# Kernel tuning notes

Hardware: AMD Instinct MI355X
Metric: run time of the kernel (lower is better)

The kernel has to match this reference:

```python
import jax, jax.numpy as jnp
from jax import lax
import numpy as np

PN_FEAT = 64


def _conv(x, w, b):
    # x: [B,H,W,Cin], w: [kh,kw,Cin,Cout] (SAME padding, stride 1)
    return lax.conv_general_dilated(x, w, (1, 1), 'SAME',
                                    dimension_numbers=('NHWC', 'HWIO', 'NHWC')) + b


def setup_inputs() -> dict:
    key = jax.random.key(0)
    ks = jax.random.split(key, 12)
    B, P, N, C = 4, 5000, 100, 8
    nx = ny = 240
    pillars = jax.random.normal(ks[0], (B, P, N, C), dtype=jnp.float32)
    pillar_idxs = jax.random.randint(ks[1], (B, P, 2), 0, nx).astype(jnp.int32)
    def lin(k, fi, fo):
        return jax.random.normal(k, (fi, fo), dtype=jnp.float32) / np.sqrt(fi).astype(np.float32)
    def cnv(k, kh, kw, ci, co):
        return jax.random.normal(k, (kh, kw, ci, co), dtype=jnp.float32) / np.sqrt(kh * kw * ci).astype(np.float32)
    return {
        'pillars': pillars,
        'pillar_idxs': pillar_idxs,
        'nx': nx,
        'ny': ny,
        # pointnet MLP: 8 -> 64 (tanh) -> 64
        'pn_w0': lin(ks[2], 8, 64), 'pn_b0': jnp.zeros((64,), jnp.float32),
        'pn_w1': lin(ks[3], 64, PN_FEAT), 'pn_b1': jnp.zeros((PN_FEAT,), jnp.float32),
        # resnet costmap CNN: 64 -> 128 (tanh) -> 128 (tanh) -> 1, relu output
        'cw0': cnv(ks[4], 3, 3, PN_FEAT, 128), 'cb0': jnp.zeros((128,), jnp.float32),
        'cw1': cnv(ks[5], 3, 3, 128, 128), 'cb1': jnp.zeros((128,), jnp.float32),
        'cw2': cnv(ks[6], 1, 1, 128, 1), 'cb2': jnp.zeros((1,), jnp.float32),
    }


def reference(pillars, pillar_idxs, nx, ny,
              pn_w0, pn_b0, pn_w1, pn_b1,
              cw0, cb0, cw1, cb1, cw2, cb2):
    VALID_THRESH = 1000000.0
    ACT_SCALE = 1.0
    # mask padded points (norm >= 1e6 means invalid)
    valid = (jnp.linalg.norm(pillars, axis=-1, keepdims=True) < VALID_THRESH).astype(pillars.dtype)
    # per-point MLP: [B,P,N,8] -> [B,P,N,F]
    h = jnp.tanh(pillars @ pn_w0 + pn_b0)
    feat = h @ pn_w1 + pn_b1
    # masked max over points in each pillar -> [B,P,F]
    pmax = jnp.max(feat * valid, axis=-2)
    # scatter pillar features into BEV pseudo-image [B,nx,ny,F]
    B = pillars.shape[0]
    bidx = jnp.arange(B)[:, None]                      # [B,1]
    img = jnp.zeros((B, nx, ny, PN_FEAT), pillars.dtype)
    img = img.at[bidx, pillar_idxs[..., 0], pillar_idxs[..., 1]].set(pmax)
    # costmap CNN head (NHWC internally; original is NCHW, same math)
    x = jnp.tanh(_conv(img, cw0, cb0))
    x = jnp.tanh(_conv(x, cw1, cb1))
    x = _conv(x, cw2, cb2)
    return jax.nn.relu(x) * ACT_SCALE            # [B,nx,ny,1]
```

## Files before the change

### kernel.cpp

```cpp
#include <hip/hip_runtime.h>
#include <hip/hip_bf16.h>
#include <math.h>

#define B  4
#define P  5000
#define NPT 100
#define F  64
#define NX 240
#define NY 240
#define C1 128

typedef __attribute__((ext_vector_type(8)))  short short8;
typedef __attribute__((ext_vector_type(16))) float f32x16;

__device__ __forceinline__ float tanh_fast(float x) {
    float e = exp2f(x * 2.8853900817779268f);
    float r = __builtin_amdgcn_rcpf(e + 1.0f);
    return __builtin_fmaf(-2.0f, r, 1.0f);
}
__device__ __forceinline__ short bf16_bits(float f) {
    return (short)(__bfloat16_as_ushort(__float2bfloat16(f)));
}
__device__ __forceinline__ void async_load16(const void* g, void* l) {
    __builtin_amdgcn_global_load_lds(
        (const __attribute__((address_space(1))) void*)g,
        (__attribute__((address_space(3))) void*)l, 16, 0, 0);
}

__global__ __launch_bounds__(128, 4) void pn_mfma_kernel(
    const float* __restrict__ pillars,
    const short* __restrict__ w0p,
    const float* __restrict__ b0,
    const __hip_bfloat16* __restrict__ w1t,
    const float* __restrict__ b1,
    float* __restrict__ pmax)
{
    constexpr int HS = F + 8;
    constexpr int XS = 40;
    __shared__ short buf[128 * HS];
    __shared__ float red[2][F];
    __shared__ unsigned int vb32[4];
    short* xA = buf;
    short* hA = buf;

    int bp = blockIdx.x;
    int n  = threadIdx.x;
    int wave = n >> 6, lane = n & 63;
    int mr = lane & 31;
    int g  = lane >> 5;
    bool live = (n < NPT);

    const float* xp = pillars + ((size_t)bp * NPT + (live ? n : 0)) * 8;
    float4 q0 = *(const float4*)xp;
    float4 q1 = *(const float4*)(xp + 4);
    float x[8] = {q0.x, q0.y, q0.z, q0.w, q1.x, q1.y, q1.z, q1.w};

    float ss = 0.f;
#pragma unroll
    for (int c = 0; c < 8; c++) ss += x[c] * x[c];
    bool valid = live && (ss < 1e12f);

    unsigned long long bal = __ballot(valid);
    if (lane == 0) {
        vb32[wave * 2]     = (unsigned)bal;
        vb32[wave * 2 + 1] = (unsigned)(bal >> 32);
    }

    short8 xhi, xlo, xz;
#pragma unroll
    for (int c = 0; c < 8; c++) {
        __hip_bfloat16 hb = __float2bfloat16(x[c]);
        float hv = __bfloat162float(hb);
        xhi[c] = (short)__bfloat16_as_ushort(hb);
        xlo[c] = bf16_bits(x[c] - hv);
        xz[c] = 0;
    }
    *(short8*)&xA[n * XS + 0]  = xhi;
    *(short8*)&xA[n * XS + 8]  = xlo;
    *(short8*)&xA[n * XS + 16] = xhi;
    *(short8*)&xA[n * XS + 24] = xz;
    __syncthreads();

    short8 wb[2][2];
#pragma unroll
    for (int kk = 0; kk < 2; kk++)
#pragma unroll
        for (int nt = 0; nt < 2; nt++)
            wb[kk][nt] = *(const short8*)(w0p + ((kk * 2 + g) * 64 + nt * 32 + mr) * 8);

    f32x16 hc00 = {0,0,0,0,0,0,0,0,0,0,0,0,0,0,0,0};
    f32x16 hc01 = hc00, hc10 = hc00, hc11 = hc00;
#pragma unroll
    for (int kk = 0; kk < 2; kk++) {
        short8 a0 = *(const short8*)&xA[(wave * 64 + mr) * XS + kk * 16 + g * 8];
        short8 a1 = *(const short8*)&xA[(wave * 64 + 32 + mr) * XS + kk * 16 + g * 8];
        hc00 = __builtin_amdgcn_mfma_f32_32x32x16_bf16(a0, wb[kk][0], hc00, 0, 0, 0);
        hc01 = __builtin_amdgcn_mfma_f32_32x32x16_bf16(a0, wb[kk][1], hc01, 0, 0, 0);
        hc10 = __builtin_amdgcn_mfma_f32_32x32x16_bf16(a1, wb[kk][0], hc10, 0, 0, 0);
        hc11 = __builtin_amdgcn_mfma_f32_32x32x16_bf16(a1, wb[kk][1], hc11, 0, 0, 0);
    }
    __syncthreads();

    float b00 = b0[mr];
    float b01 = b0[32 + mr];
#pragma unroll
    for (int mt = 0; mt < 2; mt++) {
#pragma unroll
        for (int r = 0; r < 16; r++) {
            int prow = wave * 64 + mt * 32 + (r & 3) + 8 * (r >> 2) + 4 * g;
            float h0 = (mt == 0) ? hc00[r] : hc10[r];
            float h1 = (mt == 0) ? hc01[r] : hc11[r];
            hA[prow * HS + mr]      = bf16_bits(tanh_fast(h0 + b00));
            hA[prow * HS + 32 + mr] = bf16_bits(tanh_fast(h1 + b01));
        }
    }
    __syncthreads();

    short8 bfrag[2][4];
#pragma unroll
    for (int nt = 0; nt < 2; nt++)
#pragma unroll
        for (int c0 = 0; c0 < 4; c0++)
            bfrag[nt][c0] = *(const short8*)((const short*)w1t +
                                (nt * 32 + mr) * F + c0 * 16 + g * 8);

    f32x16 acc00 = {0,0,0,0,0,0,0,0,0,0,0,0,0,0,0,0};
    f32x16 acc01 = acc00, acc10 = acc00, acc11 = acc00;

    const short* arow = &hA[(wave * 64 + mr) * HS + g * 8];
#pragma unroll
    for (int c0 = 0; c0 < 4; c0++) {
        short8 af0 = *(const short8*)(arow + c0 * 16);
        short8 af1 = *(const short8*)(arow + 32 * HS + c0 * 16);
        acc00 = __builtin_amdgcn_mfma_f32_32x32x16_bf16(af0, bfrag[0][c0], acc00, 0, 0, 0);
        acc01 = __builtin_amdgcn_mfma_f32_32x32x16_bf16(af0, bfrag[1][c0], acc01, 0, 0, 0);
        acc10 = __builtin_amdgcn_mfma_f32_32x32x16_bf16(af1, bfrag[0][c0], acc10, 0, 0, 0);
        acc11 = __builtin_amdgcn_mfma_f32_32x32x16_bf16(af1, bfrag[1][c0], acc11, 0, 0, 0);
    }

    float bv0 = b1[mr];
    float bv1 = b1[32 + mr];
    bool allv = ((vb32[0] & vb32[1] & vb32[2]) == 0xFFFFFFFFu) &&
                ((vb32[3] & 0xFu) == 0xFu);
    float mx0 = -INFINITY, mx1 = -INFINITY;

    if (allv) {
#pragma unroll
        for (int mt = 0; mt < 2; mt++) {
#pragma unroll
            for (int r = 0; r < 16; r++) {
                bool inc = !(wave == 1 && mt == 1) || (g == 0 && r < 4);
                if (inc) {
                    mx0 = fmaxf(mx0, (mt == 0) ? acc00[r] : acc10[r]);
                    mx1 = fmaxf(mx1, (mt == 0) ? acc01[r] : acc11[r]);
                }
            }
        }
        mx0 += bv0;
        mx1 += bv1;
    } else {
        unsigned wm0 = vb32[wave * 2];
        unsigned wm1 = vb32[wave * 2 + 1];
#pragma unroll
        for (int mt = 0; mt < 2; mt++) {
            unsigned wm = (mt == 0) ? wm0 : wm1;
#pragma unroll
            for (int r = 0; r < 16; r++) {
                int idx = (r & 3) + 8 * (r >> 2) + 4 * g;
                bool inc = !(wave == 1 && mt == 1) || (idx < 4);
                if (inc) {
                    bool vbit = (wm >> idx) & 1;
                    float a0 = (mt == 0) ? acc00[r] : acc10[r];
                    float a1 = (mt == 0) ? acc01[r] : acc11[r];
                    mx0 = fmaxf(mx0, vbit ? (a0 + bv0) : 0.0f);
                    mx1 = fmaxf(mx1, vbit ? (a1 + bv1) : 0.0f);
                }
            }
        }
    }
    mx0 = fmaxf(mx0, __shfl_xor(mx0, 32, 64));
    mx1 = fmaxf(mx1, __shfl_xor(mx1, 32, 64));
    if (lane < 32) { red[wave][mr] = mx0; red[wave][32 + mr] = mx1; }
    __syncthreads();
    if (n < F)
        pmax[(size_t)bp * F + n] = fmaxf(red[0][n], red[1][n]);
}

__global__ __launch_bounds__(256) void winner_kernel(
    const int* __restrict__ idxs, int* __restrict__ winner)
{
    int i = blockIdx.x * 256 + threadIdx.x;
    if (i >= B * P) return;
    int ix = idxs[i * 2], iy = idxs[i * 2 + 1];
    int b = i / P, p = i % P;
    atomicMax(&winner[(b * NX + ix) * NY + iy], p);
}

__global__ __launch_bounds__(64) void scatter_kernel(
    const int* __restrict__ idxs, const int* __restrict__ winner,
    const float* __restrict__ pmax, __hip_bfloat16* __restrict__ img)
{
    int bp = blockIdx.x;
    int f = threadIdx.x;
    int ix = idxs[bp * 2], iy = idxs[bp * 2 + 1];
    int b = bp / P, p = bp % P;
    int cell = (b * NX + ix) * NY + iy;
    if (winner[cell] == p)
        img[(size_t)cell * F + f] = __float2bfloat16(pmax[(size_t)bp * F + f]);
}

__global__ __launch_bounds__(256) void cvt_w_kernel(
    const float* __restrict__ w, __hip_bfloat16* __restrict__ wt, int cin)
{
    int idx = blockIdx.x * 256 + threadIdx.x;
    int total = 9 * cin * 128;
    if (idx >= total) return;
    int co = idx % 128;
    int rest = idx / 128;
    int ci = rest % cin;
    int t  = rest / cin;
    int c0 = ci >> 4, c16 = ci & 15;
    wt[(((size_t)(t * (cin >> 4) + c0)) * 128 + co) * 16 + c16] = __float2bfloat16(w[idx]);
}

__global__ __launch_bounds__(256) void cvt_w1_kernel(
    const float* __restrict__ w1, __hip_bfloat16* __restrict__ w1t)
{
    int idx = blockIdx.x * 256 + threadIdx.x;
    if (idx >= F * F) return;
    int k = idx >> 6, nn = idx & 63;
    w1t[nn * F + k] = __float2bfloat16(w1[idx]);
}

__global__ __launch_bounds__(256) void cvt_w0p_kernel(
    const float* __restrict__ w0, short* __restrict__ w0p)
{
    int idx = blockIdx.x * 256 + threadIdx.x;
    if (idx >= 4 * 64 * 8) return;
    int j = idx & 7;
    int nn = (idx >> 3) & 63;
    int s = idx >> 9;
    float wv = w0[j * F + nn];
    __hip_bfloat16 hb = __float2bfloat16(wv);
    short out = 0;
    if (s < 2)      out = (short)__bfloat16_as_ushort(hb);
    else if (s == 2) out = bf16_bits(wv - __bfloat162float(hb));
    w0p[idx] = out;
}

template<int CIN, bool FUSE>
__global__ __launch_bounds__(512, 2) void conv_mfma(
    const __hip_bfloat16* __restrict__ in,
    const __hip_bfloat16* __restrict__ wt,
    const float* __restrict__ bias,
    const float* __restrict__ w2,
    const float* __restrict__ b2,
    const __hip_bfloat16* __restrict__ zerobuf,
    __hip_bfloat16* __restrict__ out_bf,
    float* __restrict__ out_f)
{
    constexpr int NPASS = CIN / 32;
    constexpr int NC16  = 2;
    constexpr int CSTR  = 400;
    __shared__ short sP[2][4 * CSTR * 8];
    __shared__ float sred[FUSE ? 2 : 1][4][64];

    int tid  = threadIdx.x;
    int wave = tid >> 6;
    int lane = tid & 63;
    int mr = lane & 31;
    int g  = lane >> 5;
    int coh = wave & 1;
    int xr  = wave >> 1;
    int x0 = blockIdx.x * 4;
    int y0 = blockIdx.y * 62;
    if (y0 > 178) y0 = 178;
    int b  = blockIdx.z;
    int n0 = coh * 64;

    const short* wts = (const short*)wt;

    auto stage = [&](int pp, short* dst) {
        int gy = y0 - 1 + lane;
        bool yok = (gy >= 0 && gy < NY);
#pragma unroll
        for (int j = 0; j < 3; j++) {
            int q  = j * 8 + wave;
            int cc = q & 3;
            int dx = q >> 2;
            int gx = x0 - 1 + dx;
            const __hip_bfloat16* src =
                (yok && gx >= 0 && gx < NX)
                ? &in[(((size_t)b * NX + gx) * NY + gy) * CIN + pp * 32 + cc * 8]
                : zerobuf;
            async_load16(src, (void*)(dst + (cc * CSTR + dx * 64) * 8));
        }
    };

    f32x16 acc[2][2];
#pragma unroll
    for (int mt = 0; mt < 2; mt++)
#pragma unroll
        for (int nt = 0; nt < 2; nt++)
            acc[mt][nt] = (f32x16){0,0,0,0,0,0,0,0,0,0,0,0,0,0,0,0};

    stage(0, sP[0]);

#pragma unroll
    for (int p = 0; p < NPASS; p++) {
        __syncthreads();
        if (p + 1 < NPASS)
            stage(p + 1, sP[(p + 1) & 1]);
        const short* sPb = sP[p & 1];

#pragma unroll
        for (int tap = 0; tap < 9; tap++) {
            int kh = tap / 3, kw = tap % 3;
            int rowcol = (xr + kh) * 64 + kw;
            const short* wrow = wts + ((size_t)(tap * (CIN / 16) + p * NC16) * 128 + n0 + mr) * 16 + g * 8;
#pragma unroll
            for (int c0 = 0; c0 < NC16; c0++) {
                short8 w0f = *(const short8*)(wrow + (size_t)c0 * 2048);
                short8 w1f = *(const short8*)(wrow + (size_t)c0 * 2048 + 512);
                int cc = c0 * 2 + g;
                const short* abase = sPb + (cc * CSTR + rowcol + mr) * 8;
                short8 a0 = *(const short8*)(abase);
                short8 a1 = *(const short8*)(abase + 32 * 8);
                acc[0][0] = __builtin_amdgcn_mfma_f32_32x32x16_bf16(a0, w0f, acc[0][0], 0, 0, 0);
                acc[0][1] = __builtin_amdgcn_mfma_f32_32x32x16_bf16(a0, w1f, acc[0][1], 0, 0, 0);
                acc[1][0] = __builtin_amdgcn_mfma_f32_32x32x16_bf16(a1, w0f, acc[1][0], 0, 0, 0);
                acc[1][1] = __builtin_amdgcn_mfma_f32_32x32x16_bf16(a1, w1f, acc[1][1], 0, 0, 0);
            }
        }
    }

    float bv0 = bias[n0 + mr];
    float bv1 = bias[n0 + 32 + mr];
    if (!FUSE) {
        size_t base = ((size_t)b * NX + (x0 + xr)) * NY;
#pragma unroll
        for (int mt = 0; mt < 2; mt++) {
#pragma unroll
            for (int r = 0; r < 16; r++) {
                int row = mt * 32 + (r & 3) + 8 * (r >> 2) + 4 * g;
                if (row < 62) {
                    int y = y0 + row;
                    out_bf[(base + y) * C1 + n0 + mr]      = __float2bfloat16(tanh_fast(acc[mt][0][r] + bv0));
                    out_bf[(base + y) * C1 + n0 + 32 + mr] = __float2bfloat16(tanh_fast(acc[mt][1][r] + bv1));
                }
            }
        }
    } else {
        float w20 = w2[n0 + mr];
        float w21 = w2[n0 + 32 + mr];
#pragma unroll
        for (int mt = 0; mt < 2; mt++) {
#pragma unroll
            for (int r = 0; r < 16; r++) {
                float v = tanh_fast(acc[mt][0][r] + bv0) * w20
                        + tanh_fast(acc[mt][1][r] + bv1) * w21;
                v += __shfl_xor(v, 1, 64);
                v += __shfl_xor(v, 2, 64);
                v += __shfl_xor(v, 4, 64);
                v += __shfl_xor(v, 8, 64);
                v += __shfl_xor(v, 16, 64);
                if (mr == 0)
                    sred[coh][xr][mt * 32 + (r & 3) + 8 * (r >> 2) + 4 * g] = v;
            }
        }
        __syncthreads();
        if (tid < 256) {
            int xr2 = tid >> 6;
            int yy  = tid & 63;
            if (yy < 62) {
                float r = sred[0][xr2][yy] + sred[1][xr2][yy] + b2[0];
                out_f[((size_t)b * NX + (x0 + xr2)) * NY + (y0 + yy)] = fmaxf(r, 0.f);
            }
        }
    }
}

extern "C" void kernel_launch(void* const* d_in, const int* in_sizes, int n_in,
                              void* d_out, int out_size, void* d_ws, size_t ws_size,
                              hipStream_t stream) {
    const float* pillars = (const float*)d_in[0];
    const int*   idxs    = (const int*)d_in[1];
    const float* pn_w0   = (const float*)d_in[4];
    const float* pn_b0   = (const float*)d_in[5];
    const float* pn_w1   = (const float*)d_in[6];
    const float* pn_b1   = (const float*)d_in[7];
    const float* cw0     = (const float*)d_in[8];
    const float* cb0     = (const float*)d_in[9];
    const float* cw1     = (const float*)d_in[10];
    const float* cb1     = (const float*)d_in[11];
    const float* cw2     = (const float*)d_in[12];
    const float* cb2     = (const float*)d_in[13];
    float* out = (float*)d_out;

    char* ws = (char*)d_ws;
    const size_t IMG_BYTES  = (size_t)B * NX * NY * F * 2;
    const size_t OUT1_BYTES = (size_t)B * NX * NY * C1 * 2;
    const size_t WIN_BYTES  = (size_t)B * NX * NY * 4;
    const size_t PMAX_BYTES = (size_t)B * P * F * 4;
    const size_t WT1_BYTES  = (size_t)9 * C1 * F * 2;
    const size_t WT2_BYTES  = (size_t)9 * C1 * C1 * 2;
    const size_t W1T_BYTES  = (size_t)F * F * 2;
    const size_t W0P_BYTES  = (size_t)4 * 64 * 8 * 2;
    __hip_bfloat16* img  = (__hip_bfloat16*)ws;
    __hip_bfloat16* out1 = (__hip_bfloat16*)(ws + IMG_BYTES);
    int*   winner = (int*)(ws + IMG_BYTES + OUT1_BYTES);
    float* pmax   = (float*)(ws + IMG_BYTES + OUT1_BYTES + WIN_BYTES);
    __hip_bfloat16* wt1 = (__hip_bfloat16*)(ws + IMG_BYTES + OUT1_BYTES + WIN_BYTES + PMAX_BYTES);
    __hip_bfloat16* wt2 = (__hip_bfloat16*)(ws + IMG_BYTES + OUT1_BYTES + WIN_BYTES + PMAX_BYTES + WT1_BYTES);
    __hip_bfloat16* w1t = (__hip_bfloat16*)(ws + IMG_BYTES + OUT1_BYTES + WIN_BYTES + PMAX_BYTES + WT1_BYTES + WT2_BYTES);
    short* w0p = (short*)(ws + IMG_BYTES + OUT1_BYTES + WIN_BYTES + PMAX_BYTES + WT1_BYTES + WT2_BYTES + W1T_BYTES);
    __hip_bfloat16* zerobuf = (__hip_bfloat16*)(ws + IMG_BYTES + OUT1_BYTES + WIN_BYTES + PMAX_BYTES + WT1_BYTES + WT2_BYTES + W1T_BYTES + W0P_BYTES);

    hipMemsetAsync(img, 0, IMG_BYTES, stream);
    hipMemsetAsync(winner, 0xFF, WIN_BYTES, stream);
    hipMemsetAsync(zerobuf, 0, 64, stream);

    cvt_w_kernel<<<(9 * F * C1 + 255) / 256, 256, 0, stream>>>(cw0, wt1, F);
    cvt_w_kernel<<<(9 * C1 * C1 + 255) / 256, 256, 0, stream>>>(cw1, wt2, C1);
    cvt_w1_kernel<<<(F * F + 255) / 256, 256, 0, stream>>>(pn_w1, w1t);
    cvt_w0p_kernel<<<(4 * 64 * 8 + 255) / 256, 256, 0, stream>>>(pn_w0, w0p);

    pn_mfma_kernel<<<B * P, 128, 0, stream>>>(pillars, w0p, pn_b0, w1t, pn_b1, pmax);
    winner_kernel<<<(B * P + 255) / 256, 256, 0, stream>>>(idxs, winner);
    scatter_kernel<<<B * P, 64, 0, stream>>>(idxs, winner, pmax, img);

    conv_mfma<F, false><<<dim3(NX / 4, 4, B), 512, 0, stream>>>(
        img, wt1, cb0, nullptr, nullptr, zerobuf, out1, nullptr);
    conv_mfma<C1, true><<<dim3(NX / 4, 4, B), 512, 0, stream>>>(
        out1, wt2, cb1, cw2, cb2, zerobuf, nullptr, out);
}
```

Baseline: 338.6 us.

## Fuse pillar scatter into PointNet kernel and keep hidden activations in registers

```diff
diff --git a/kernel.cpp b/kernel.cpp
--- a/kernel.cpp
+++ b/kernel.cpp
@@ -27,21 +27,19 @@
         (__attribute__((address_space(3))) void*)l, 16, 0, 0);
 }
 
-__global__ __launch_bounds__(128, 4) void pn_mfma_kernel(
+__global__ __launch_bounds__(128, 2) void pn_mfma_kernel(
     const float* __restrict__ pillars,
     const short* __restrict__ w0p,
-    const float* __restrict__ b0,
     const __hip_bfloat16* __restrict__ w1t,
     const float* __restrict__ b1,
-    float* __restrict__ pmax)
-{
-    constexpr int HS = F + 8;
+    const int* __restrict__ idxs,
+    const int* __restrict__ winner,
+    __hip_bfloat16* __restrict__ img)
+{
     constexpr int XS = 40;
-    __shared__ short buf[128 * HS];
+    __shared__ short xA[128 * XS];
     __shared__ float red[2][F];
     __shared__ unsigned int vb32[4];
-    short* xA = buf;
-    short* hA = buf;
 
     int bp = blockIdx.x;
     int n  = threadIdx.x;
@@ -66,55 +64,60 @@
         vb32[wave * 2 + 1] = (unsigned)(bal >> 32);
     }
 
-    short8 xhi, xlo, xz;
+    short8 xhi, xlo, xone;
 #pragma unroll
     for (int c = 0; c < 8; c++) {
         __hip_bfloat16 hb = __float2bfloat16(x[c]);
         float hv = __bfloat162float(hb);
         xhi[c] = (short)__bfloat16_as_ushort(hb);
         xlo[c] = bf16_bits(x[c] - hv);
-        xz[c] = 0;
+        xone[c] = (c < 2) ? bf16_bits(1.0f) : (short)0;
     }
     *(short8*)&xA[n * XS + 0]  = xhi;
     *(short8*)&xA[n * XS + 8]  = xlo;
     *(short8*)&xA[n * XS + 16] = xhi;
-    *(short8*)&xA[n * XS + 24] = xz;
+    *(short8*)&xA[n * XS + 24] = xone;
     __syncthreads();
 
     short8 wb[2][2];
 #pragma unroll
     for (int kk = 0; kk < 2; kk++)
 #pragma unroll
-        for (int nt = 0; nt < 2; nt++)
-            wb[kk][nt] = *(const short8*)(w0p + ((kk * 2 + g) * 64 + nt * 32 + mr) * 8);
-
-    f32x16 hc00 = {0,0,0,0,0,0,0,0,0,0,0,0,0,0,0,0};
-    f32x16 hc01 = hc00, hc10 = hc00, hc11 = hc00;
+        for (int m = 0; m < 2; m++)
+            wb[kk][m] = *(const short8*)(w0p + ((kk * 2 + g) * 64 + m * 32 + mr) * 8);
+
+    f32x16 acc1[2][2];
+#pragma unroll
+    for (int ptt = 0; ptt < 2; ptt++)
+#pragma unroll
+        for (int m = 0; m < 2; m++)
+            acc1[ptt][m] = (f32x16){0,0,0,0,0,0,0,0,0,0,0,0,0,0,0,0};
+
 #pragma unroll
     for (int kk = 0; kk < 2; kk++) {
-        short8 a0 = *(const short8*)&xA[(wave * 64 + mr) * XS + kk * 16 + g * 8];
-        short8 a1 = *(const short8*)&xA[(wave * 64 + 32 + mr) * XS + kk * 16 + g * 8];
-        hc00 = __builtin_amdgcn_mfma_f32_32x32x16_bf16(a0, wb[kk][0], hc00, 0, 0, 0);
-        hc01 = __builtin_amdgcn_mfma_f32_32x32x16_bf16(a0, wb[kk][1], hc01, 0, 0, 0);
-        hc10 = __builtin_amdgcn_mfma_f32_32x32x16_bf16(a1, wb[kk][0], hc10, 0, 0, 0);
-        hc11 = __builtin_amdgcn_mfma_f32_32x32x16_bf16(a1, wb[kk][1], hc11, 0, 0, 0);
-    }
-    __syncthreads();
-
-    float b00 = b0[mr];
-    float b01 = b0[32 + mr];
-#pragma unroll
-    for (int mt = 0; mt < 2; mt++) {
-#pragma unroll
-        for (int r = 0; r < 16; r++) {
-            int prow = wave * 64 + mt * 32 + (r & 3) + 8 * (r >> 2) + 4 * g;
-            float h0 = (mt == 0) ? hc00[r] : hc10[r];
-            float h1 = (mt == 0) ? hc01[r] : hc11[r];
-            hA[prow * HS + mr]      = bf16_bits(tanh_fast(h0 + b00));
-            hA[prow * HS + 32 + mr] = bf16_bits(tanh_fast(h1 + b01));
-        }
-    }
-    __syncthreads();
+        short8 x0 = *(const short8*)&xA[(wave * 64 + mr) * XS + kk * 16 + g * 8];
+        short8 x1 = *(const short8*)&xA[(wave * 64 + 32 + mr) * XS + kk * 16 + g * 8];
+        acc1[0][0] = __builtin_amdgcn_mfma_f32_32x32x16_bf16(wb[kk][0], x0, acc1[0][0], 0, 0, 0);
+        acc1[0][1] = __builtin_amdgcn_mfma_f32_32x32x16_bf16(wb[kk][1], x0, acc1[0][1], 0, 0, 0);
+        acc1[1][0] = __builtin_amdgcn_mfma_f32_32x32x16_bf16(wb[kk][0], x1, acc1[1][0], 0, 0, 0);
+        acc1[1][1] = __builtin_amdgcn_mfma_f32_32x32x16_bf16(wb[kk][1], x1, acc1[1][1], 0, 0, 0);
+    }
+
+    short8 afrag[2][4];
+#pragma unroll
+    for (int ptt = 0; ptt < 2; ptt++) {
+#pragma unroll
+        for (int c0 = 0; c0 < 4; c0++) {
+            short8 t;
+#pragma unroll
+            for (int j = 0; j < 8; j++) {
+                float v = (c0 >> 1) ? acc1[ptt][1][8 * (c0 & 1) + j]
+                                    : acc1[ptt][0][8 * (c0 & 1) + j];
+                t[j] = bf16_bits(tanh_fast(v));
+            }
+            afrag[ptt][c0] = t;
+        }
+    }
 
     short8 bfrag[2][4];
 #pragma unroll
@@ -124,18 +127,19 @@
             bfrag[nt][c0] = *(const short8*)((const short*)w1t +
                                 (nt * 32 + mr) * F + c0 * 16 + g * 8);
 
-    f32x16 acc00 = {0,0,0,0,0,0,0,0,0,0,0,0,0,0,0,0};
-    f32x16 acc01 = acc00, acc10 = acc00, acc11 = acc00;
-
-    const short* arow = &hA[(wave * 64 + mr) * HS + g * 8];
+    f32x16 a2[2][2];
+#pragma unroll
+    for (int ptt = 0; ptt < 2; ptt++)
+#pragma unroll
+        for (int nt = 0; nt < 2; nt++)
+            a2[ptt][nt] = (f32x16){0,0,0,0,0,0,0,0,0,0,0,0,0,0,0,0};
+
 #pragma unroll
     for (int c0 = 0; c0 < 4; c0++) {
-        short8 af0 = *(const short8*)(arow + c0 * 16);
-        short8 af1 = *(const short8*)(arow + 32 * HS + c0 * 16);
-        acc00 = __builtin_amdgcn_mfma_f32_32x32x16_bf16(af0, bfrag[0][c0], acc00, 0, 0, 0);
-        acc01 = __builtin_amdgcn_mfma_f32_32x32x16_bf16(af0, bfrag[1][c0], acc01, 0, 0, 0);
-        acc10 = __builtin_amdgcn_mfma_f32_32x32x16_bf16(af1, bfrag[0][c0], acc10, 0, 0, 0);
-        acc11 = __builtin_amdgcn_mfma_f32_32x32x16_bf16(af1, bfrag[1][c0], acc11, 0, 0, 0);
+        a2[0][0] = __builtin_amdgcn_mfma_f32_32x32x16_bf16(afrag[0][c0], bfrag[0][c0], a2[0][0], 0, 0, 0);
+        a2[0][1] = __builtin_amdgcn_mfma_f32_32x32x16_bf16(afrag[0][c0], bfrag[1][c0], a2[0][1], 0, 0, 0);
+        a2[1][0] = __builtin_amdgcn_mfma_f32_32x32x16_bf16(afrag[1][c0], bfrag[0][c0], a2[1][0], 0, 0, 0);
+        a2[1][1] = __builtin_amdgcn_mfma_f32_32x32x16_bf16(afrag[1][c0], bfrag[1][c0], a2[1][1], 0, 0, 0);
     }
 
     float bv0 = b1[mr];
@@ -146,13 +150,13 @@
 
     if (allv) {
 #pragma unroll
-        for (int mt = 0; mt < 2; mt++) {
+        for (int ptt = 0; ptt < 2; ptt++) {
 #pragma unroll
             for (int r = 0; r < 16; r++) {
-                bool inc = !(wave == 1 && mt == 1) || (g == 0 && r < 4);
+                bool inc = !(wave == 1 && ptt == 1) || (g == 0 && r < 4);
                 if (inc) {
-                    mx0 = fmaxf(mx0, (mt == 0) ? acc00[r] : acc10[r]);
-                    mx1 = fmaxf(mx1, (mt == 0) ? acc01[r] : acc11[r]);
+                    mx0 = fmaxf(mx0, (ptt == 0) ? a2[0][0][r] : a2[1][0][r]);
+                    mx1 = fmaxf(mx1, (ptt == 0) ? a2[0][1][r] : a2[1][1][r]);
                 }
             }
         }
@@ -162,16 +166,16 @@
         unsigned wm0 = vb32[wave * 2];
         unsigned wm1 = vb32[wave * 2 + 1];
 #pragma unroll
-        for (int mt = 0; mt < 2; mt++) {
-            unsigned wm = (mt == 0) ? wm0 : wm1;
+        for (int ptt = 0; ptt < 2; ptt++) {
+            unsigned wm = (ptt == 0) ? wm0 : wm1;
 #pragma unroll
             for (int r = 0; r < 16; r++) {
                 int idx = (r & 3) + 8 * (r >> 2) + 4 * g;
-                bool inc = !(wave == 1 && mt == 1) || (idx < 4);
+                bool inc = !(wave == 1 && ptt == 1) || (idx < 4);
                 if (inc) {
                     bool vbit = (wm >> idx) & 1;
-                    float a0 = (mt == 0) ? acc00[r] : acc10[r];
-                    float a1 = (mt == 0) ? acc01[r] : acc11[r];
+                    float a0 = (ptt == 0) ? a2[0][0][r] : a2[1][0][r];
+                    float a1 = (ptt == 0) ? a2[0][1][r] : a2[1][1][r];
                     mx0 = fmaxf(mx0, vbit ? (a0 + bv0) : 0.0f);
                     mx1 = fmaxf(mx1, vbit ? (a1 + bv1) : 0.0f);
                 }
@@ -182,8 +186,14 @@
     mx1 = fmaxf(mx1, __shfl_xor(mx1, 32, 64));
     if (lane < 32) { red[wave][mr] = mx0; red[wave][32 + mr] = mx1; }
     __syncthreads();
-    if (n < F)
-        pmax[(size_t)bp * F + n] = fmaxf(red[0][n], red[1][n]);
+    if (n < F) {
+        float v = fmaxf(red[0][n], red[1][n]);
+        int ix = idxs[bp * 2], iy = idxs[bp * 2 + 1];
+        int b = bp / P, p = bp % P;
+        int cell = (b * NX + ix) * NY + iy;
+        if (winner[cell] == p)
+            img[(size_t)cell * F + n] = __float2bfloat16(v);
+    }
 }
 
 __global__ __launch_bounds__(256) void winner_kernel(
@@ -194,19 +204,6 @@
     int ix = idxs[i * 2], iy = idxs[i * 2 + 1];
     int b = i / P, p = i % P;
     atomicMax(&winner[(b * NX + ix) * NY + iy], p);
-}
-
-__global__ __launch_bounds__(64) void scatter_kernel(
-    const int* __restrict__ idxs, const int* __restrict__ winner,
-    const float* __restrict__ pmax, __hip_bfloat16* __restrict__ img)
-{
-    int bp = blockIdx.x;
-    int f = threadIdx.x;
-    int ix = idxs[bp * 2], iy = idxs[bp * 2 + 1];
-    int b = bp / P, p = bp % P;
-    int cell = (b * NX + ix) * NY + iy;
-    if (winner[cell] == p)
-        img[(size_t)cell * F + f] = __float2bfloat16(pmax[(size_t)bp * F + f]);
 }
 
 __global__ __launch_bounds__(256) void cvt_w_kernel(
@@ -228,23 +225,33 @@
 {
     int idx = blockIdx.x * 256 + threadIdx.x;
     if (idx >= F * F) return;
-    int k = idx >> 6, nn = idx & 63;
-    w1t[nn * F + k] = __float2bfloat16(w1[idx]);
+    int nn = idx >> 6, kk = idx & 63;
+    int c0 = kk >> 4, g = (kk >> 3) & 1, j = kk & 7;
+    int k = 16 * c0 + 4 * g + (j & 3) + 8 * (j >> 2);
+    w1t[nn * F + kk] = __float2bfloat16(w1[k * F + nn]);
 }
 
 __global__ __launch_bounds__(256) void cvt_w0p_kernel(
-    const float* __restrict__ w0, short* __restrict__ w0p)
+    const float* __restrict__ w0, const float* __restrict__ b0,
+    short* __restrict__ w0p)
 {
     int idx = blockIdx.x * 256 + threadIdx.x;
     if (idx >= 4 * 64 * 8) return;
     int j = idx & 7;
     int nn = (idx >> 3) & 63;
     int s = idx >> 9;
-    float wv = w0[j * F + nn];
-    __hip_bfloat16 hb = __float2bfloat16(wv);
     short out = 0;
-    if (s < 2)      out = (short)__bfloat16_as_ushort(hb);
-    else if (s == 2) out = bf16_bits(wv - __bfloat162float(hb));
+    if (s < 3) {
+        float wv = w0[j * F + nn];
+        __hip_bfloat16 hb = __float2bfloat16(wv);
+        if (s < 2)      out = (short)__bfloat16_as_ushort(hb);
+        else            out = bf16_bits(wv - __bfloat162float(hb));
+    } else {
+        float bv = b0[nn];
+        __hip_bfloat16 hb = __float2bfloat16(bv);
+        if (j == 0)      out = (short)__bfloat16_as_ushort(hb);
+        else if (j == 1) out = bf16_bits(bv - __bfloat162float(hb));
+    }
     w0p[idx] = out;
 }
 
@@ -409,7 +416,6 @@
     __hip_bfloat16* img  = (__hip_bfloat16*)ws;
     __hip_bfloat16* out1 = (__hip_bfloat16*)(ws + IMG_BYTES);
     int*   winner = (int*)(ws + IMG_BYTES + OUT1_BYTES);
-    float* pmax   = (float*)(ws + IMG_BYTES + OUT1_BYTES + WIN_BYTES);
     __hip_bfloat16* wt1 = (__hip_bfloat16*)(ws + IMG_BYTES + OUT1_BYTES + WIN_BYTES + PMAX_BYTES);
     __hip_bfloat16* wt2 = (__hip_bfloat16*)(ws + IMG_BYTES + OUT1_BYTES + WIN_BYTES + PMAX_BYTES + WT1_BYTES);
     __hip_bfloat16* w1t = (__hip_bfloat16*)(ws + IMG_BYTES + OUT1_BYTES + WIN_BYTES + PMAX_BYTES + WT1_BYTES + WT2_BYTES);
@@ -423,11 +429,11 @@
     cvt_w_kernel<<<(9 * F * C1 + 255) / 256, 256, 0, stream>>>(cw0, wt1, F);
     cvt_w_kernel<<<(9 * C1 * C1 + 255) / 256, 256, 0, stream>>>(cw1, wt2, C1);
     cvt_w1_kernel<<<(F * F + 255) / 256, 256, 0, stream>>>(pn_w1, w1t);
-    cvt_w0p_kernel<<<(4 * 64 * 8 + 255) / 256, 256, 0, stream>>>(pn_w0, w0p);
-
-    pn_mfma_kernel<<<B * P, 128, 0, stream>>>(pillars, w0p, pn_b0, w1t, pn_b1, pmax);
+    cvt_w0p_kernel<<<(4 * 64 * 8 + 255) / 256, 256, 0, stream>>>(pn_w0, pn_b0, w0p);
+
     winner_kernel<<<(B * P + 255) / 256, 256, 0, stream>>>(idxs, winner);
-    scatter_kernel<<<B * P, 64, 0, stream>>>(idxs, winner, pmax, img);
+    pn_mfma_kernel<<<B * P, 128, 0, stream>>>(pillars, w0p, w1t, pn_b1,
+                                              idxs, winner, img);
 
     conv_mfma<F, false><<<dim3(NX / 4, 4, B), 512, 0, stream>>>(
         img, wt1, cb0, nullptr, nullptr, zerobuf, out1, nullptr);
```

Result: faster. 325.1 us (-4.0%).
